# Performance work log

Hardware: AMD Instinct MI355X
Metric: run time of the kernel (lower is better)

The kernel has to match this reference:

```python
import jax, jax.numpy as jnp
import numpy as np

BATCH, SEQ, DMODEL, DHID = 4, 4096, 1024, 1024
R_MIN, R_MAX = 0.9, 0.99
MAX_PHASE = np.pi / 50  # module overrides ctor arg with pi/50
EPS = 1e-5


def setup_inputs() -> dict:
    key = jax.random.key(0)
    ks = jax.random.split(key, 8)
    # nu_init
    u1 = jax.random.uniform(ks[0], (DHID,)) * (1 - EPS) + EPS
    mag_sq = u1 * (R_MAX ** 2 - R_MIN ** 2) + R_MIN ** 2
    nu_log = jnp.log(-0.5 * jnp.log(mag_sq + EPS))
    # theta_init
    u2 = jax.random.uniform(ks[1], (DHID,)) * (1 - EPS) + EPS
    theta_log = jnp.log(MAX_PHASE * u2)
    B_re = jax.random.normal(ks[2], (DHID, DMODEL)) / np.sqrt(2 * DMODEL)
    B_im = jax.random.normal(ks[3], (DHID, DMODEL)) / np.sqrt(2 * DMODEL)
    C_re = jax.random.normal(ks[4], (DMODEL, DHID)) / np.sqrt(DHID)
    C_im = jax.random.normal(ks[5], (DMODEL, DHID)) / np.sqrt(DHID)
    D_skip = jax.random.normal(ks[6], (DMODEL,))
    inputs = jax.random.normal(ks[7], (BATCH, SEQ, DMODEL), dtype=jnp.float32)
    return {"inputs": inputs, "nu_log": nu_log, "theta_log": theta_log,
            "B_re": B_re, "B_im": B_im, "C_re": C_re, "C_im": C_im,
            "D_skip": D_skip}


def reference(inputs, nu_log, theta_log, B_re, B_im, C_re, C_im, D_skip):
    nu = jnp.exp(nu_log)
    theta = jnp.exp(theta_log)
    diag_lambda = jnp.exp(-nu + 1j * theta)            # [H] complex
    # forward recomputes gamma_log from nu_log (parameter gamma_log unused)
    gamma_log = 0.5 * jnp.log(1 - jnp.exp(-2 * jnp.exp(nu_log)) + EPS)
    B_norm = (B_re + 1j * B_im) * jnp.exp(gamma_log)[:, None]  # [H, D]
    inputs_c = inputs.astype(jnp.complex64)
    Bu = jnp.einsum('hd,btd->bth', B_norm, inputs_c)   # [B, T, H]

    def step(h, bu_t):
        h = diag_lambda * h + bu_t
        return h, h

    h0 = jnp.zeros((inputs.shape[0], diag_lambda.shape[0]), dtype=Bu.dtype)
    _, hs = jax.lax.scan(step, h0, jnp.swapaxes(Bu, 0, 1))  # [T, B, H]
    hs = jnp.swapaxes(hs, 0, 1)                              # [B, T, H]
    C_complex = C_re + 1j * C_im                              # [D, H]
    out = jnp.einsum('bth,dh->btd', hs, C_complex).real + inputs * D_skip
    return out.astype(jnp.float32)
```

## Files before the change

### kernel.cpp

```cpp
#include <hip/hip_runtime.h>


typedef __bf16 bf16x8 __attribute__((ext_vector_type(8)));
typedef float floatx4 __attribute__((ext_vector_type(4)));

__device__ __forceinline__ unsigned short f2bf(float f) {
  unsigned u = __float_as_uint(f);
  u += 0x7fffu + ((u >> 16) & 1u);
  return (unsigned short)(u >> 16);
}
__device__ __forceinline__ float bf2f(unsigned short s) {
  return __uint_as_float(((unsigned)s) << 16);
}


__global__ void prep_params(const float* __restrict__ nu_log,
                            const float* __restrict__ theta_log,
                            float* __restrict__ lam,
                            float* __restrict__ lamL,
                            float* __restrict__ gamma)
{
  int h = blockIdx.x * 256 + threadIdx.x;
  float nu = expf(nu_log[h]);
  float th = expf(theta_log[h]);
  float r = expf(-nu);
  lam[h]        = r * cosf(th);
  lam[1024 + h] = r * sinf(th);
  float rL = expf(-128.0f * nu);
  lamL[h]        = rL * cosf(128.0f * th);
  lamL[1024 + h] = rL * sinf(128.0f * th);
  gamma[h] = sqrtf(1.0f - expf(-2.0f * nu) + 1e-5f);
}

__global__ void prep_B(const float* __restrict__ B_re, const float* __restrict__ B_im,
                       const float* __restrict__ gamma, unsigned short* __restrict__ Bcat)
{
  int tid = blockIdx.x * 256 + threadIdx.x;
  int n = tid >> 10;
  int d = tid & 1023;
  int h = n & 1023;
  float v = (n < 1024 ? B_re[h * 1024 + d] : B_im[h * 1024 + d]) * gamma[h];
  Bcat[tid] = f2bf(v);
}

__global__ void prep_C(const float* __restrict__ C_re, const float* __restrict__ C_im,
                       unsigned short* __restrict__ Ccat)
{
  int tid = blockIdx.x * 256 + threadIdx.x;
  int d = tid >> 11;
  int k = tid & 2047;
  float v = (k < 1024) ? C_re[d * 1024 + k] : -C_im[d * 1024 + (k - 1024)];
  Ccat[tid] = f2bf(v);
}

__global__ void conv_inputs(const float* __restrict__ in, unsigned short* __restrict__ outb)
{
  int tid = blockIdx.x * 256 + threadIdx.x;
  float4 v = ((const float4*)in)[tid];
  unsigned lo = (unsigned)f2bf(v.x) | ((unsigned)f2bf(v.y) << 16);
  unsigned hi = (unsigned)f2bf(v.z) | ((unsigned)f2bf(v.w) << 16);
  ((uint2*)outb)[tid] = make_uint2(lo, hi);
}


template <int EPI>
__global__ __launch_bounds__(256) void gemm_bt_kernel(
    const unsigned short* __restrict__ A,
    const unsigned short* __restrict__ Bt,
    void* __restrict__ Cout,
    int M, int N, int K,
    const float* __restrict__ skip_in,
    const float* __restrict__ skip_w)
{
  __shared__ unsigned short As[128 * 32];
  __shared__ unsigned short Bs[128 * 32];

  const int tid  = threadIdx.x;
  const int lane = tid & 63;
  const int wave = tid >> 6;
  const int wm = wave >> 1;
  const int wn = wave & 1;

  const int flat    = blockIdx.x;
  const int xcd     = flat & 7;
  const int local   = flat >> 3;
  const int m_tile  = xcd * 16 + (local & 15);
  const int n_tile  = local >> 4;
  const int m0 = m_tile * 128;
  const int n0 = n_tile * 128;

  const int ldr = lane >> 2;
  const int pos = lane & 3;
  const int lm  = lane & 15;
  const int q   = lane >> 4;

  floatx4 acc[4][4];
#pragma unroll
  for (int i = 0; i < 4; ++i)
#pragma unroll
    for (int j = 0; j < 4; ++j)
      acc[i][j] = (floatx4){0.f, 0.f, 0.f, 0.f};

  for (int kt = 0; kt < K; kt += 32) {
    __syncthreads();
#pragma unroll
    for (int half = 0; half < 2; ++half) {
      const int r  = wave * 32 + half * 16 + ldr;
      const int ca = pos ^ ((r >> 1) & 3);
      const unsigned short* ga = A  + (size_t)(m0 + r) * K + kt + ca * 8;
      const unsigned short* gb = Bt + (size_t)(n0 + r) * K + kt + ca * 8;
      __builtin_amdgcn_global_load_lds(
          (const __attribute__((address_space(1))) void*)ga,
          (__attribute__((address_space(3))) void*)&As[r * 32 + pos * 8], 16, 0, 0);
      __builtin_amdgcn_global_load_lds(
          (const __attribute__((address_space(1))) void*)gb,
          (__attribute__((address_space(3))) void*)&Bs[r * 32 + pos * 8], 16, 0, 0);
    }
    __syncthreads();

    bf16x8 afrag[4], bfrag[4];
#pragma unroll
    for (int i = 0; i < 4; ++i) {
      const int r = wm * 64 + i * 16 + lm;
      afrag[i] = *reinterpret_cast<const bf16x8*>(&As[r * 32 + (q ^ ((r >> 1) & 3)) * 8]);
    }
#pragma unroll
    for (int j = 0; j < 4; ++j) {
      const int r = wn * 64 + j * 16 + lm;
      bfrag[j] = *reinterpret_cast<const bf16x8*>(&Bs[r * 32 + (q ^ ((r >> 1) & 3)) * 8]);
    }
#pragma unroll
    for (int i = 0; i < 4; ++i)
#pragma unroll
      for (int j = 0; j < 4; ++j)
        acc[i][j] = __builtin_amdgcn_mfma_f32_16x16x32_bf16(afrag[i], bfrag[j], acc[i][j], 0, 0, 0);
  }

#pragma unroll
  for (int i = 0; i < 4; ++i) {
#pragma unroll
    for (int j = 0; j < 4; ++j) {
      const int row0 = m0 + wm * 64 + i * 16 + q * 4;
      const int col  = n0 + wn * 64 + j * 16 + lm;
#pragma unroll
      for (int r = 0; r < 4; ++r) {
        const size_t idx = (size_t)(row0 + r) * N + col;
        if (EPI == 0) {
          ((unsigned short*)Cout)[idx] = f2bf(acc[i][j][r]);
        } else {
          ((float*)Cout)[idx] = acc[i][j][r] + skip_in[idx] * skip_w[col];
        }
      }
    }
  }
}


__global__ void scan_finals(const unsigned short* __restrict__ Bu,
                            const float* __restrict__ lam,
                            float2* __restrict__ finals)
{
  int tid = blockIdx.x * 256 + threadIdx.x;
  int h = tid & 1023, c = (tid >> 10) & 31, b = tid >> 15;
  float lre = lam[h], lim = lam[1024 + h];
  const unsigned short* p = Bu + ((size_t)(b * 4096 + c * 128) * 2048) + h;
  float yre = 0.f, yim = 0.f;
#pragma unroll 4
  for (int t = 0; t < 128; ++t) {
    float ure = bf2f(p[0]);
    float uim = bf2f(p[1024]);
    float nre = fmaf(lre, yre, fmaf(-lim, yim, ure));
    float nim = fmaf(lre, yim, fmaf(lim, yre, uim));
    yre = nre; yim = nim;
    p += 2048;
  }
  finals[tid] = make_float2(yre, yim);
}

__global__ void scan_carries(const float2* __restrict__ finals,
                             const float* __restrict__ lamL,
                             float2* __restrict__ carry)
{
  int tid = blockIdx.x * 256 + threadIdx.x;
  int h = tid & 1023, b = tid >> 10;
  float Lre = lamL[h], Lim = lamL[1024 + h];
  float Hre = 0.f, Him = 0.f;
  for (int c = 0; c < 32; ++c) {
    size_t i = ((size_t)(b * 32 + c) << 10) + h;
    carry[i] = make_float2(Hre, Him);
    float2 f = finals[i];
    float nre = fmaf(Lre, Hre, fmaf(-Lim, Him, f.x));
    float nim = fmaf(Lre, Him, fmaf(Lim, Hre, f.y));
    Hre = nre; Him = nim;
  }
}

__global__ void scan_apply(const float* __restrict__ lam,
                           const float2* __restrict__ carry,
                           unsigned short* __restrict__ Bu)
{
  int tid = blockIdx.x * 256 + threadIdx.x;
  int h = tid & 1023, c = (tid >> 10) & 31, b = tid >> 15;
  float lre = lam[h], lim = lam[1024 + h];
  float2 cv = carry[tid];
  float yre = cv.x, yim = cv.y;
  unsigned short* p = Bu + ((size_t)(b * 4096 + c * 128) * 2048) + h;
#pragma unroll 4
  for (int t = 0; t < 128; ++t) {
    float ure = bf2f(p[0]);
    float uim = bf2f(p[1024]);
    float nre = fmaf(lre, yre, fmaf(-lim, yim, ure));
    float nim = fmaf(lre, yim, fmaf(lim, yre, uim));
    yre = nre; yim = nim;
    p[0]    = f2bf(yre);
    p[1024] = f2bf(yim);
    p += 2048;
  }
}


extern "C" void kernel_launch(void* const* d_in, const int* in_sizes, int n_in,
                              void* d_out, int out_size, void* d_ws, size_t ws_size,
                              hipStream_t stream)
{
  const float* inputs    = (const float*)d_in[0];
  const float* nu_log    = (const float*)d_in[1];
  const float* theta_log = (const float*)d_in[2];
  const float* B_re      = (const float*)d_in[3];
  const float* B_im      = (const float*)d_in[4];
  const float* C_re      = (const float*)d_in[5];
  const float* C_im      = (const float*)d_in[6];
  const float* D_skip    = (const float*)d_in[7];
  float* out = (float*)d_out;

  char* ws = (char*)d_ws;
  float* lam   = (float*)ws;
  float* lamL  = lam + 2048;
  float* gamma = lamL + 2048;
  unsigned short* inp_bf = (unsigned short*)(ws + (1 << 16));
  unsigned short* Bcat   = inp_bf + (size_t)16384 * 1024;
  unsigned short* Ccat   = Bcat   + (size_t)2048 * 1024;
  unsigned short* Bu     = Ccat   + (size_t)1024 * 2048;
  float2* finals = (float2*)(Bu + (size_t)16384 * 2048);
  float2* carry  = finals + 131072;

  prep_params<<<4,    256, 0, stream>>>(nu_log, theta_log, lam, lamL, gamma);
  prep_B     <<<8192, 256, 0, stream>>>(B_re, B_im, gamma, Bcat);
  prep_C     <<<8192, 256, 0, stream>>>(C_re, C_im, Ccat);
  conv_inputs<<<16384,256, 0, stream>>>(inputs, inp_bf);

  gemm_bt_kernel<0><<<2048, 256, 0, stream>>>(
      inp_bf, Bcat, Bu, 16384, 2048, 1024, nullptr, nullptr);

  scan_finals <<<512, 256, 0, stream>>>(Bu, lam, finals);
  scan_carries<<<16,  256, 0, stream>>>(finals, lamL, carry);
  scan_apply  <<<512, 256, 0, stream>>>(lam, carry, Bu);

  gemm_bt_kernel<1><<<1024, 256, 0, stream>>>(
      Bu, Ccat, out, 16384, 1024, 2048, inputs, D_skip);
}
```

Baseline: 382.4 us.

## Double-buffer LDS tiles in bf16 GEMM to overlap global loads with MFMA

Splits the shared-memory A and B tiles into two buffers. The next K-slice is prefetched with global_load_lds into the spare buffer while MFMAs run on the current one. Tile addresses are precomputed outside the loop, and one of the two barriers per iteration is removed. The aim is to hide global-memory latency in both GEMMs, at the cost of twice the LDS per block, which may lower occupancy.

```diff
diff --git a/kernel.cpp b/kernel.cpp
--- a/kernel.cpp
+++ b/kernel.cpp
@@ -72,8 +72,8 @@
     const float* __restrict__ skip_in,
     const float* __restrict__ skip_w)
 {
-  __shared__ unsigned short As[128 * 32];
-  __shared__ unsigned short Bs[128 * 32];
+  __shared__ unsigned short As[2][128 * 32];
+  __shared__ unsigned short Bs[2][128 * 32];
 
   const int tid  = threadIdx.x;
   const int lane = tid & 63;
@@ -94,6 +94,18 @@
   const int lm  = lane & 15;
   const int q   = lane >> 4;
 
+  const int r0 = wave * 32 + ldr;
+  const int ca0 = pos ^ ((r0 >> 1) & 3);
+  const int r1 = r0 + 16;
+  const int ca1 = pos ^ ((r1 >> 1) & 3);
+
+  const unsigned short* gA0 = A  + (size_t)(m0 + r0) * K + ca0 * 8;
+  const unsigned short* gA1 = A  + (size_t)(m0 + r1) * K + ca1 * 8;
+  const unsigned short* gB0 = Bt + (size_t)(n0 + r0) * K + ca0 * 8;
+  const unsigned short* gB1 = Bt + (size_t)(n0 + r1) * K + ca1 * 8;
+  const int lofs0 = r0 * 32 + pos * 8;
+  const int lofs1 = r1 * 32 + pos * 8;
+
   floatx4 acc[4][4];
 #pragma unroll
   for (int i = 0; i < 4; ++i)
@@ -101,39 +113,60 @@
     for (int j = 0; j < 4; ++j)
       acc[i][j] = (floatx4){0.f, 0.f, 0.f, 0.f};
 
+  {
+    __builtin_amdgcn_global_load_lds(
+        (const __attribute__((address_space(1))) void*)gA0,
+        (__attribute__((address_space(3))) void*)&As[0][lofs0], 16, 0, 0);
+    __builtin_amdgcn_global_load_lds(
+        (const __attribute__((address_space(1))) void*)gA1,
+        (__attribute__((address_space(3))) void*)&As[0][lofs1], 16, 0, 0);
+    __builtin_amdgcn_global_load_lds(
+        (const __attribute__((address_space(1))) void*)gB0,
+        (__attribute__((address_space(3))) void*)&Bs[0][lofs0], 16, 0, 0);
+    __builtin_amdgcn_global_load_lds(
+        (const __attribute__((address_space(1))) void*)gB1,
+        (__attribute__((address_space(3))) void*)&Bs[0][lofs1], 16, 0, 0);
+  }
+
+  int cur = 0;
   for (int kt = 0; kt < K; kt += 32) {
     __syncthreads();
-#pragma unroll
-    for (int half = 0; half < 2; ++half) {
-      const int r  = wave * 32 + half * 16 + ldr;
-      const int ca = pos ^ ((r >> 1) & 3);
-      const unsigned short* ga = A  + (size_t)(m0 + r) * K + kt + ca * 8;
-      const unsigned short* gb = Bt + (size_t)(n0 + r) * K + kt + ca * 8;
-      __builtin_amdgcn_global_load_lds(
-          (const __attribute__((address_space(1))) void*)ga,
-          (__attribute__((address_space(3))) void*)&As[r * 32 + pos * 8], 16, 0, 0);
-      __builtin_amdgcn_global_load_lds(
-          (const __attribute__((address_space(1))) void*)gb,
-          (__attribute__((address_space(3))) void*)&Bs[r * 32 + pos * 8], 16, 0, 0);
-    }
-    __syncthreads();
+
+    const int nxt = cur ^ 1;
+    if (kt + 32 < K) {
+      const int ko = kt + 32;
+      __builtin_amdgcn_global_load_lds(
+          (const __attribute__((address_space(1))) void*)(gA0 + ko),
+          (__attribute__((address_space(3))) void*)&As[nxt][lofs0], 16, 0, 0);
+      __builtin_amdgcn_global_load_lds(
+          (const __attribute__((address_space(1))) void*)(gA1 + ko),
+          (__attribute__((address_space(3))) void*)&As[nxt][lofs1], 16, 0, 0);
+      __builtin_amdgcn_global_load_lds(
+          (const __attribute__((address_space(1))) void*)(gB0 + ko),
+          (__attribute__((address_space(3))) void*)&Bs[nxt][lofs0], 16, 0, 0);
+      __builtin_amdgcn_global_load_lds(
+          (const __attribute__((address_space(1))) void*)(gB1 + ko),
+          (__attribute__((address_space(3))) void*)&Bs[nxt][lofs1], 16, 0, 0);
+    }
 
     bf16x8 afrag[4], bfrag[4];
 #pragma unroll
     for (int i = 0; i < 4; ++i) {
       const int r = wm * 64 + i * 16 + lm;
-      afrag[i] = *reinterpret_cast<const bf16x8*>(&As[r * 32 + (q ^ ((r >> 1) & 3)) * 8]);
+      afrag[i] = *reinterpret_cast<const bf16x8*>(&As[cur][r * 32 + (q ^ ((r >> 1) & 3)) * 8]);
     }
 #pragma unroll
     for (int j = 0; j < 4; ++j) {
       const int r = wn * 64 + j * 16 + lm;
-      bfrag[j] = *reinterpret_cast<const bf16x8*>(&Bs[r * 32 + (q ^ ((r >> 1) & 3)) * 8]);
+      bfrag[j] = *reinterpret_cast<const bf16x8*>(&Bs[cur][r * 32 + (q ^ ((r >> 1) & 3)) * 8]);
     }
 #pragma unroll
     for (int i = 0; i < 4; ++i)
 #pragma unroll
       for (int j = 0; j < 4; ++j)
         acc[i][j] = __builtin_amdgcn_mfma_f32_16x16x32_bf16(afrag[i], bfrag[j], acc[i][j], 0, 0, 0);
+
+    cur = nxt;
   }
 
 #pragma unroll
```

Result: faster. 364.2 us (-4.7%).

## Double-buffer B tile in LDS and stream A fragments directly into registers

Applied to the files above, without the earlier changes.

The GEMM kernel now keeps only the B operand in LDS, double-buffered so the next k-slice is prefetched while MFMAs run on the current one, with one barrier per step instead of two. A fragments are loaded straight from global memory into registers one step ahead, which drops A's LDS staging. The cost is that the two column waves each fetch the same A data, doubling A's global/L2 traffic and adding register pressure. Correctness also depends on the async LDS loads having finished by the next barrier.

```diff
diff --git a/kernel.cpp b/kernel.cpp
--- a/kernel.cpp
+++ b/kernel.cpp
@@ -63,6 +63,36 @@
 }
 
 
+#define GEMM_STEP(KT, CUR, NXT, ACUR, ANEXT)                                     \
+  {                                                                              \
+    __syncthreads();                                                             \
+    if ((KT) + 32 < K) {                                                         \
+      const int ko = (KT) + 32;                                                  \
+      __builtin_amdgcn_global_load_lds(                                          \
+          (const __attribute__((address_space(1))) void*)(gB0 + ko),             \
+          (__attribute__((address_space(3))) void*)&Bs[NXT][lofs0], 16, 0, 0);   \
+      __builtin_amdgcn_global_load_lds(                                          \
+          (const __attribute__((address_space(1))) void*)(gB1 + ko),             \
+          (__attribute__((address_space(3))) void*)&Bs[NXT][lofs1], 16, 0, 0);   \
+      _Pragma("unroll")                                                          \
+      for (int i = 0; i < 4; ++i)                                                \
+        ANEXT[i] = *reinterpret_cast<const bf16x8*>(gAf + (size_t)(i * 16) * K + ko); \
+    }                                                                            \
+    bf16x8 bfrag[4];                                                             \
+    _Pragma("unroll")                                                            \
+    for (int j = 0; j < 4; ++j) {                                                \
+      const int r = wn * 64 + j * 16 + lm;                                       \
+      bfrag[j] = *reinterpret_cast<const bf16x8*>(                               \
+          &Bs[CUR][r * 32 + (q ^ ((r >> 1) & 3)) * 8]);                          \
+    }                                                                            \
+    _Pragma("unroll")                                                            \
+    for (int i = 0; i < 4; ++i)                                                  \
+      _Pragma("unroll")                                                          \
+      for (int j = 0; j < 4; ++j)                                                \
+        acc[i][j] = __builtin_amdgcn_mfma_f32_16x16x32_bf16(ACUR[i], bfrag[j],   \
+                                                            acc[i][j], 0, 0, 0); \
+  }
+
 template <int EPI>
 __global__ __launch_bounds__(256) void gemm_bt_kernel(
     const unsigned short* __restrict__ A,
@@ -72,8 +102,7 @@
     const float* __restrict__ skip_in,
     const float* __restrict__ skip_w)
 {
-  __shared__ unsigned short As[128 * 32];
-  __shared__ unsigned short Bs[128 * 32];
+  __shared__ unsigned short Bs[2][128 * 32];
 
   const int tid  = threadIdx.x;
   const int lane = tid & 63;
@@ -94,6 +123,17 @@
   const int lm  = lane & 15;
   const int q   = lane >> 4;
 
+  const int r0 = wave * 32 + ldr;
+  const int ca0 = pos ^ ((r0 >> 1) & 3);
+  const int r1 = r0 + 16;
+  const int ca1 = pos ^ ((r1 >> 1) & 3);
+  const unsigned short* gB0 = Bt + (size_t)(n0 + r0) * K + ca0 * 8;
+  const unsigned short* gB1 = Bt + (size_t)(n0 + r1) * K + ca1 * 8;
+  const int lofs0 = r0 * 32 + pos * 8;
+  const int lofs1 = r1 * 32 + pos * 8;
+
+  const unsigned short* gAf = A + (size_t)(m0 + wm * 64 + lm) * K + q * 8;
+
   floatx4 acc[4][4];
 #pragma unroll
   for (int i = 0; i < 4; ++i)
@@ -101,39 +141,20 @@
     for (int j = 0; j < 4; ++j)
       acc[i][j] = (floatx4){0.f, 0.f, 0.f, 0.f};
 
-  for (int kt = 0; kt < K; kt += 32) {
-    __syncthreads();
-#pragma unroll
-    for (int half = 0; half < 2; ++half) {
-      const int r  = wave * 32 + half * 16 + ldr;
-      const int ca = pos ^ ((r >> 1) & 3);
-      const unsigned short* ga = A  + (size_t)(m0 + r) * K + kt + ca * 8;
-      const unsigned short* gb = Bt + (size_t)(n0 + r) * K + kt + ca * 8;
-      __builtin_amdgcn_global_load_lds(
-          (const __attribute__((address_space(1))) void*)ga,
-          (__attribute__((address_space(3))) void*)&As[r * 32 + pos * 8], 16, 0, 0);
-      __builtin_amdgcn_global_load_lds(
-          (const __attribute__((address_space(1))) void*)gb,
-          (__attribute__((address_space(3))) void*)&Bs[r * 32 + pos * 8], 16, 0, 0);
-    }
-    __syncthreads();
-
-    bf16x8 afrag[4], bfrag[4];
-#pragma unroll
-    for (int i = 0; i < 4; ++i) {
-      const int r = wm * 64 + i * 16 + lm;
-      afrag[i] = *reinterpret_cast<const bf16x8*>(&As[r * 32 + (q ^ ((r >> 1) & 3)) * 8]);
-    }
-#pragma unroll
-    for (int j = 0; j < 4; ++j) {
-      const int r = wn * 64 + j * 16 + lm;
-      bfrag[j] = *reinterpret_cast<const bf16x8*>(&Bs[r * 32 + (q ^ ((r >> 1) & 3)) * 8]);
-    }
-#pragma unroll
-    for (int i = 0; i < 4; ++i)
-#pragma unroll
-      for (int j = 0; j < 4; ++j)
-        acc[i][j] = __builtin_amdgcn_mfma_f32_16x16x32_bf16(afrag[i], bfrag[j], acc[i][j], 0, 0, 0);
+  __builtin_amdgcn_global_load_lds(
+      (const __attribute__((address_space(1))) void*)gB0,
+      (__attribute__((address_space(3))) void*)&Bs[0][lofs0], 16, 0, 0);
+  __builtin_amdgcn_global_load_lds(
+      (const __attribute__((address_space(1))) void*)gB1,
+      (__attribute__((address_space(3))) void*)&Bs[0][lofs1], 16, 0, 0);
+  bf16x8 a0[4], a1[4];
+#pragma unroll
+  for (int i = 0; i < 4; ++i)
+    a0[i] = *reinterpret_cast<const bf16x8*>(gAf + (size_t)(i * 16) * K);
+
+  for (int kt = 0; kt < K; kt += 64) {
+    GEMM_STEP(kt,      0, 1, a0, a1);
+    GEMM_STEP(kt + 32, 1, 0, a1, a0);
   }
 
 #pragma unroll
```

Result: slower. 468.3 us (+22.5%).
